# Optimization experiments

Measured on AMD Instinct MI355X. Metric: run time of the kernel, lower is better.

## Reference

```python
import jax, jax.numpy as jnp
import numpy as np

N, IN, OUT = 128, 1024, 1024
STE_TEMP = 1.0


def setup_inputs() -> dict:
    key = jax.random.key(0)
    k1, k2 = jax.random.split(key)
    x = jax.random.normal(k1, (N, IN), dtype=jnp.float32)
    # nn.init.uniform_(weight, -0.5, 0.5)
    weight = jax.random.uniform(k2, (OUT, IN), dtype=jnp.float32, minval=-0.5, maxval=0.5)
    bias = jnp.zeros((OUT,), dtype=jnp.float32)
    return {"x": x, "weight": weight, "bias": bias}


def reference(x, weight, bias):
    # scores: [N, out, in] = W[out,in] broadcast-added to x[N,1,in]
    scores = weight[None, :, :] + x[:, None, :]
    # training-mode forward: hard max value, STE blend with softmax-weighted smooth value
    hard = jnp.max(jax.lax.stop_gradient(scores), axis=-1)          # [N, out]
    soft_w = jax.nn.softmax(scores / STE_TEMP, axis=-1)              # [N, out, in]
    soft = jnp.sum(soft_w * scores, axis=-1)                          # [N, out]
    out = hard + (soft - jax.lax.stop_gradient(soft))
    return out + bias
```

## Files before the change

### kernel.cpp

```cpp
#include <hip/hip_runtime.h>

#define N_ROWS 128
#define IN_DIM 1024
#define OUT_DIM 1024


__global__ __launch_bounds__(256, 2)
void tropical_linear_kernel(const float* __restrict__ x,
                            const float* __restrict__ w,
                            const float* __restrict__ bias,
                            float* __restrict__ out) {
    __shared__ float4 xs[8 * 256];

    const int tid  = threadIdx.x;
    const int wid  = tid >> 6;
    const int lane = tid & 63;
    const int g    = lane & 7;
    const int og   = lane >> 3;

    const int bn = blockIdx.x >> 5;
    const int bo = blockIdx.x & 31;
    const int n0 = bn * 8;
    const int o  = bo * 32 + wid * 8 + og;

    const float4* __restrict__ x4 = (const float4*)x;

#pragma unroll
    for (int i = 0; i < 8; ++i) {
        const int idx = tid + i * 256;
        const int r = idx >> 8, c = idx & 255;
        xs[idx] = x4[(size_t)(n0 + r) * 256 + c];
    }
    __syncthreads();

    float acc[8];
#pragma unroll
    for (int j = 0; j < 8; ++j) acc[j] = -3.4e38f;

    const float4* __restrict__ wr = (const float4*)(w + (size_t)o * IN_DIM);

    float4 wb[4];
#pragma unroll
    for (int i = 0; i < 4; ++i) wb[i] = wr[i * 8 + g];

    for (int tt = 0; tt < 8; ++tt) {
        float4 wc[4];
#pragma unroll
        for (int i = 0; i < 4; ++i) wc[i] = wb[i];
        if (tt < 7) {
#pragma unroll
            for (int i = 0; i < 4; ++i) wb[i] = wr[(tt + 1) * 32 + i * 8 + g];
        }
#pragma unroll
        for (int i = 0; i < 4; ++i) {
            const int kq = tt * 32 + i * 8 + g;
#pragma unroll
            for (int j = 0; j < 8; ++j) {
                const float4 xv = xs[j * 256 + kq];
                const float s0 = wc[i].x + xv.x;
                const float s1 = wc[i].y + xv.y;
                const float s2 = wc[i].z + xv.z;
                const float s3 = wc[i].w + xv.w;
                const float m = fmaxf(fmaxf(s0, s1), s2);
                acc[j] = fmaxf(fmaxf(m, s3), acc[j]);
            }
        }
    }

#pragma unroll
    for (int j = 0; j < 8; ++j) {
        float v = acc[j];
        v = fmaxf(v, __shfl_xor(v, 1, 64));
        v = fmaxf(v, __shfl_xor(v, 2, 64));
        v = fmaxf(v, __shfl_xor(v, 4, 64));
        acc[j] = v;
    }

    if (g == 0) {
        const float b = bias[o];
#pragma unroll
        for (int j = 0; j < 8; ++j) {
            out[(size_t)(n0 + j) * OUT_DIM + o] = acc[j] + b;
        }
    }
}

extern "C" void kernel_launch(void* const* d_in, const int* in_sizes, int n_in,
                              void* d_out, int out_size, void* d_ws, size_t ws_size,
                              hipStream_t stream) {
    const float* x    = (const float*)d_in[0];
    const float* w    = (const float*)d_in[1];
    const float* bias = (const float*)d_in[2];
    float* out = (float*)d_out;

    dim3 grid(512);
    dim3 block(256);
    hipLaunchKernelGGL(tropical_linear_kernel, grid, block, 0, stream, x, w, bias, out);
}
```

Baseline: 69.93 us.

## Register-block four output columns per thread to reuse x loads across columns

```diff
diff --git a/kernel.cpp b/kernel.cpp
--- a/kernel.cpp
+++ b/kernel.cpp
@@ -5,7 +5,7 @@
 #define OUT_DIM 1024
 
 
-__global__ __launch_bounds__(256, 2)
+__global__ __launch_bounds__(128, 1)
 void tropical_linear_kernel(const float* __restrict__ x,
                             const float* __restrict__ w,
                             const float* __restrict__ bias,
@@ -15,72 +15,84 @@
     const int tid  = threadIdx.x;
     const int wid  = tid >> 6;
     const int lane = tid & 63;
-    const int g    = lane & 7;
-    const int og   = lane >> 3;
+    const int g    = lane & 15;
+    const int og   = lane >> 4;
 
     const int bn = blockIdx.x >> 5;
     const int bo = blockIdx.x & 31;
     const int n0 = bn * 8;
-    const int o  = bo * 32 + wid * 8 + og;
+    const int ob = bo * 32 + wid * 16;
 
     const float4* __restrict__ x4 = (const float4*)x;
 
 #pragma unroll
-    for (int i = 0; i < 8; ++i) {
-        const int idx = tid + i * 256;
+    for (int i = 0; i < 16; ++i) {
+        const int idx = tid + i * 128;
         const int r = idx >> 8, c = idx & 255;
         xs[idx] = x4[(size_t)(n0 + r) * 256 + c];
     }
     __syncthreads();
 
-    float acc[8];
+    float acc[4][8];
 #pragma unroll
-    for (int j = 0; j < 8; ++j) acc[j] = -3.4e38f;
+    for (int c = 0; c < 4; ++c)
+#pragma unroll
+        for (int j = 0; j < 8; ++j) acc[c][j] = -3.4e38f;
 
-    const float4* __restrict__ wr = (const float4*)(w + (size_t)o * IN_DIM);
+    const float4* __restrict__ wr[4];
+#pragma unroll
+    for (int c = 0; c < 4; ++c)
+        wr[c] = (const float4*)(w + (size_t)(ob + c * 4 + og) * IN_DIM);
 
-    float4 wb[4];
+    float4 wcur[4], wnxt[4];
 #pragma unroll
-    for (int i = 0; i < 4; ++i) wb[i] = wr[i * 8 + g];
+    for (int c = 0; c < 4; ++c) wcur[c] = wr[c][g];
 
-    for (int tt = 0; tt < 8; ++tt) {
-        float4 wc[4];
+#pragma unroll 2
+    for (int t = 0; t < 16; ++t) {
+        if (t < 15) {
 #pragma unroll
-        for (int i = 0; i < 4; ++i) wc[i] = wb[i];
-        if (tt < 7) {
+            for (int c = 0; c < 4; ++c) wnxt[c] = wr[c][(t + 1) * 16 + g];
+        }
+        const int kq = t * 16 + g;
 #pragma unroll
-            for (int i = 0; i < 4; ++i) wb[i] = wr[(tt + 1) * 32 + i * 8 + g];
+        for (int j = 0; j < 8; ++j) {
+            const float4 xv = xs[j * 256 + kq];
+#pragma unroll
+            for (int c = 0; c < 4; ++c) {
+                const float s0 = wcur[c].x + xv.x;
+                const float s1 = wcur[c].y + xv.y;
+                const float s2 = wcur[c].z + xv.z;
+                const float s3 = wcur[c].w + xv.w;
+                const float m = fmaxf(fmaxf(s0, s1), s2);
+                acc[c][j] = fmaxf(fmaxf(m, s3), acc[c][j]);
+            }
         }
 #pragma unroll
-        for (int i = 0; i < 4; ++i) {
-            const int kq = tt * 32 + i * 8 + g;
-#pragma unroll
-            for (int j = 0; j < 8; ++j) {
-                const float4 xv = xs[j * 256 + kq];
-                const float s0 = wc[i].x + xv.x;
-                const float s1 = wc[i].y + xv.y;
-                const float s2 = wc[i].z + xv.z;
-                const float s3 = wc[i].w + xv.w;
-                const float m = fmaxf(fmaxf(s0, s1), s2);
-                acc[j] = fmaxf(fmaxf(m, s3), acc[j]);
-            }
-        }
+        for (int c = 0; c < 4; ++c) wcur[c] = wnxt[c];
     }
 
 #pragma unroll
-    for (int j = 0; j < 8; ++j) {
-        float v = acc[j];
-        v = fmaxf(v, __shfl_xor(v, 1, 64));
-        v = fmaxf(v, __shfl_xor(v, 2, 64));
-        v = fmaxf(v, __shfl_xor(v, 4, 64));
-        acc[j] = v;
-    }
+    for (int c = 0; c < 4; ++c)
+#pragma unroll
+        for (int j = 0; j < 8; ++j) {
+            float v = acc[c][j];
+            v = fmaxf(v, __shfl_xor(v, 1, 64));
+            v = fmaxf(v, __shfl_xor(v, 2, 64));
+            v = fmaxf(v, __shfl_xor(v, 4, 64));
+            v = fmaxf(v, __shfl_xor(v, 8, 64));
+            acc[c][j] = v;
+        }
 
     if (g == 0) {
-        const float b = bias[o];
 #pragma unroll
-        for (int j = 0; j < 8; ++j) {
-            out[(size_t)(n0 + j) * OUT_DIM + o] = acc[j] + b;
+        for (int c = 0; c < 4; ++c) {
+            const int o = ob + c * 4 + og;
+            const float b = bias[o];
+#pragma unroll
+            for (int j = 0; j < 8; ++j) {
+                out[(size_t)(n0 + j) * OUT_DIM + o] = acc[c][j] + b;
+            }
         }
     }
 }
@@ -94,6 +106,6 @@
     float* out = (float*)d_out;
 
     dim3 grid(512);
-    dim3 block(256);
+    dim3 block(128);
     hipLaunchKernelGGL(tropical_linear_kernel, grid, block, 0, stream, x, w, bias, out);
 }
```

After: 73.34 us. +4.9%, slower.
